# Optimization experiments

Hardware: AMD Instinct MI355X
Metric: run time of the kernel (lower is better)

Reference implementation:

```python
import jax, jax.numpy as jnp
import numpy as np

N_NODES = 100000
N_EDGES = 1600000
D_IN = 64
D_OUT = 64
K_PLUS = 3
ALPHA = 0.5
EXPONENT = -0.25


def _dir_norm_edge_weights(row, col, n, exponent):
    # directed_norm: D_out^exp A D_in^exp, zero-degree -> 0 weight
    ones = jnp.ones(row.shape[0], dtype=jnp.float32)
    out_deg = jax.ops.segment_sum(ones, row, num_segments=n)
    in_deg = jax.ops.segment_sum(ones, col, num_segments=n)
    out_inv = jnp.where(out_deg > 0, jnp.power(jnp.maximum(out_deg, 1.0), exponent), 0.0)
    in_inv = jnp.where(in_deg > 0, jnp.power(jnp.maximum(in_deg, 1.0), exponent), 0.0)
    return out_inv[row] * in_inv[col]


def _spmm(w, x, out_idx, gather_idx, n):
    # y[out_idx] += w * x[gather_idx]
    return jax.ops.segment_sum(w[:, None] * x[gather_idx], out_idx, num_segments=n)


def setup_inputs() -> dict:
    key = jax.random.key(0)
    ks = jax.random.split(key, 7)
    x_real = jax.random.normal(ks[0], (N_NODES, D_IN), dtype=jnp.float32)
    x_imag = jax.random.normal(ks[1], (N_NODES, D_IN), dtype=jnp.float32)
    edge_index = jax.random.randint(ks[2], (2, N_EDGES), 0, N_NODES, dtype=jnp.int32)
    s = 1.0 / np.sqrt(D_IN)
    W_real = jax.random.normal(ks[3], (K_PLUS, D_OUT, D_IN), dtype=jnp.float32) * s
    b_real = jax.random.normal(ks[4], (K_PLUS, D_OUT), dtype=jnp.float32) * s
    W_imag = jax.random.normal(ks[5], (K_PLUS, D_OUT, D_IN), dtype=jnp.float32) * s
    b_imag = jax.random.normal(ks[6], (K_PLUS, D_OUT), dtype=jnp.float32) * s
    return {"x_real": x_real, "x_imag": x_imag, "edge_index": edge_index,
            "W_real": W_real, "b_real": b_real, "W_imag": W_imag, "b_imag": b_imag}


def reference(x_real, x_imag, edge_index, W_real, b_real, W_imag, b_imag):
    n = x_real.shape[0]
    row, col = edge_index[0], edge_index[1]
    # adj_norm edge weights; adj_t_norm weights are identical scalars per edge
    # (in/out degrees swap under transpose), only the scatter direction differs.
    w = _dir_norm_edge_weights(row, col, n, EXPONENT)

    y_real = _spmm(w, x_real, row, col, n)    # adj_norm @ x_real
    y_imag = _spmm(w, x_imag, row, col, n)    # adj_norm @ x_imag
    y_real_t = _spmm(w, x_real, col, row, n)  # adj_t_norm @ x_real
    y_imag_t = _spmm(w, x_imag, col, row, n)  # adj_t_norm @ x_imag

    def lin_r(y):  # [K, N, O] per-order real linear
        return jnp.einsum('nd,kod->kno', y, W_real) + b_real[:, None, :]

    def lin_i(y):
        return jnp.einsum('nd,kod->kno', y, W_imag) + b_imag[:, None, :]

    coeffs = (0.5 ** jnp.arange(K_PLUS, dtype=jnp.float32))[:, None, None]  # exp penalty, i=0 -> 1

    lr_yr, li_yr = lin_r(y_real), lin_i(y_real)
    lr_yi, li_yi = lin_r(y_imag), lin_i(y_imag)
    lr_yrt, li_yrt = lin_r(y_real_t), lin_i(y_real_t)
    lr_yit, li_yit = lin_r(y_imag_t), lin_i(y_imag_t)

    sum_real_s2d = jnp.sum((lr_yr - li_yi) * coeffs, axis=0)
    sum_imag_s2d = jnp.sum((li_yr + lr_yi) * coeffs, axis=0)
    sum_real_d2s = jnp.sum((lr_yrt - li_yit) * coeffs, axis=0)
    # NOTE: faithful to original source, which uses y_real (not y_real_t) here.
    sum_imag_d2s = jnp.sum((li_yr + lr_yit) * coeffs, axis=0)

    total_real = ALPHA * sum_real_s2d + (1.0 - ALPHA) * sum_real_d2s
    total_imag = ALPHA * sum_imag_s2d + (1.0 - ALPHA) * sum_imag_d2s
    return total_real, total_imag
```

## Files before the change

kernel.cpp:

```cpp
#include <hip/hip_runtime.h>
#include <hip/hip_fp16.h>


constexpr int D = 64;
constexpr int SB = 256;
constexpr int G1 = 256;

typedef _Float16 f16x8 __attribute__((ext_vector_type(8)));
typedef float f32x4 __attribute__((ext_vector_type(4)));

__device__ __forceinline__ float2 h2_to_f2(uint p) {
  __half2 h = *(__half2*)&p;
  return __half22float2(h);
}


__global__ __launch_bounds__(256) void part_count(
    const int* __restrict__ row, const int* __restrict__ col,
    int* __restrict__ hout, int* __restrict__ hin, int E, int NBUK, int CH) {
  __shared__ int ho[256], hi_[256];
  int t = threadIdx.x, g = blockIdx.x;
  ho[t] = 0;
  hi_[t] = 0;
  __syncthreads();
  int e0 = g * CH, e1 = min(E, e0 + CH);
  for (int e = e0 + t; e < e1; e += 256) {
    atomicAdd(&ho[row[e] >> 9], 1);
    atomicAdd(&hi_[col[e] >> 9], 1);
  }
  __syncthreads();
  if (t < NBUK) {
    hout[t * G1 + g] = ho[t];
    hin[t * G1 + g] = hi_[t];
  }
}

__global__ __launch_bounds__(256) void part_scatter(
    const int* __restrict__ row, const int* __restrict__ col,
    const int* __restrict__ hout, const int* __restrict__ hin,
    uint* __restrict__ pout, uint* __restrict__ pin, int E, int NBUK, int CH) {
  __shared__ int co[256], ci[256];
  int t = threadIdx.x, g = blockIdx.x;
  if (t < NBUK) {
    co[t] = hout[t * G1 + g];
    ci[t] = hin[t * G1 + g];
  }
  __syncthreads();
  int e0 = g * CH, e1 = min(E, e0 + CH);
  for (int e = e0 + t; e < e1; e += 256) {
    int r = row[e], c = col[e];
    int po = atomicAdd(&co[r >> 9], 1);
    pout[po] = ((uint)(r & 511) << 17) | (uint)c;
    int pi = atomicAdd(&ci[c >> 9], 1);
    pin[pi] = ((uint)(c & 511) << 17) | (uint)r;
  }
}

__global__ __launch_bounds__(256) void bucket_degree(
    const uint* __restrict__ pout, const uint* __restrict__ pin,
    const int* __restrict__ hout, const int* __restrict__ hin,
    int* __restrict__ deg_out, int* __restrict__ deg_in, int E, int NBUK, int N) {
  const uint* p = blockIdx.y ? pin : pout;
  const int* h = blockIdx.y ? hin : hout;
  int* deg = blockIdx.y ? deg_in : deg_out;
  __shared__ int ld[512];
  int t = threadIdx.x, b = blockIdx.x;
  ld[t] = 0;
  ld[t + 256] = 0;
  __syncthreads();
  int s = h[b * G1];
  int e = (b + 1 < NBUK) ? h[(b + 1) * G1] : E;
  for (int j = s + t; j < e; j += 256) atomicAdd(&ld[p[j] >> 17], 1);
  __syncthreads();
  int n0 = (b << 9) + t;
  if (n0 < N) deg[n0] = ld[t];
  if (n0 + 256 < N) deg[n0 + 256] = ld[t + 256];
}

__global__ __launch_bounds__(256) void bucket_fill(
    const uint* __restrict__ pout, const uint* __restrict__ pin,
    const int* __restrict__ hout, const int* __restrict__ hin,
    const int* __restrict__ ofs_out, const int* __restrict__ ofs_in,
    const float* __restrict__ inv_out, const float* __restrict__ inv_in,
    uint* __restrict__ idx_out, uint* __restrict__ idx_in, int E, int NBUK, int N) {
  const uint* p = blockIdx.y ? pin : pout;
  const int* h = blockIdx.y ? hin : hout;
  const int* ofs = blockIdx.y ? ofs_in : ofs_out;
  const float* invnb = blockIdx.y ? inv_out : inv_in;
  uint* idx = blockIdx.y ? idx_in : idx_out;
  __shared__ int cur[512];
  int t = threadIdx.x, b = blockIdx.x;
  int n0 = (b << 9) + t;
  cur[t] = (n0 < N) ? ofs[n0] : 0;
  cur[t + 256] = (n0 + 256 < N) ? ofs[n0 + 256] : 0;
  __syncthreads();
  int s = h[b * G1];
  int e = (b + 1 < NBUK) ? h[(b + 1) * G1] : E;
  for (int j = s + t; j < e; j += 256) {
    uint pk = p[j];
    uint nbr = pk & 0x1FFFFu;
    uint hb = (uint)__half_as_ushort(__float2half(invnb[nbr]));
    int pos = atomicAdd(&cur[pk >> 17], 1);
    idx[pos] = (hb << 17) | nbr;
  }
}


__global__ __launch_bounds__(SB) void bsum_kernel(
    const int* __restrict__ a0, const int* __restrict__ a1,
    int* __restrict__ bsum, int n, int NB) {
  const int* a = blockIdx.y ? a1 : a0;
  int i = blockIdx.x * SB + threadIdx.x;
  int d = (i < n) ? a[i] : 0;
#pragma unroll
  for (int m = 1; m < 64; m <<= 1) d += __shfl_xor(d, m);
  __shared__ int ws[SB / 64];
  if ((threadIdx.x & 63) == 0) ws[threadIdx.x >> 6] = d;
  __syncthreads();
  if (threadIdx.x == 0) {
    int s = 0;
#pragma unroll
    for (int w = 0; w < SB / 64; ++w) s += ws[w];
    bsum[blockIdx.y * NB + blockIdx.x] = s;
  }
}

__global__ __launch_bounds__(1024) void bscan_kernel(int* __restrict__ bsum, int NB) {
  __shared__ int s0[1024], s1[1024];
  int t = threadIdx.x;
  int o0 = (t < NB) ? bsum[t] : 0;
  int o1 = (t < NB) ? bsum[NB + t] : 0;
  s0[t] = o0;
  s1[t] = o1;
  __syncthreads();
  for (int off = 1; off < 1024; off <<= 1) {
    int v0 = (t >= off) ? s0[t - off] : 0;
    int v1 = (t >= off) ? s1[t - off] : 0;
    __syncthreads();
    s0[t] += v0;
    s1[t] += v1;
    __syncthreads();
  }
  if (t < NB) {
    bsum[t] = s0[t] - o0;
    bsum[NB + t] = s1[t] - o1;
  }
}

__global__ __launch_bounds__(SB) void gfin_kernel(
    int* __restrict__ h0, int* __restrict__ h1,
    const int* __restrict__ bsum, int n, int NB) {
  int* h = blockIdx.y ? h1 : h0;
  int base = bsum[blockIdx.y * NB + blockIdx.x];
  int lane = threadIdx.x & 63, wv = threadIdx.x >> 6;
  int i = blockIdx.x * SB + threadIdx.x;
  int d = (i < n) ? h[i] : 0;
  int sc = d;
#pragma unroll
  for (int off = 1; off < 64; off <<= 1) {
    int v = __shfl_up(sc, off);
    if (lane >= off) sc += v;
  }
  __shared__ int ws[SB / 64];
  if (lane == 63) ws[wv] = sc;
  __syncthreads();
  int wbase = 0;
#pragma unroll
  for (int w = 0; w < SB / 64; ++w)
    if (w < wv) wbase += ws[w];
  if (i < n) h[i] = base + wbase + (sc - d);
}

__global__ __launch_bounds__(SB) void sfin_kernel(
    const int* __restrict__ deg_out, const int* __restrict__ deg_in,
    const int* __restrict__ bsum,
    int* __restrict__ ofs_out, int* __restrict__ ofs_in,
    float* __restrict__ inv_out, float* __restrict__ inv_in, int N, int NB) {
  const int* deg = blockIdx.y ? deg_in : deg_out;
  int* ofs = blockIdx.y ? ofs_in : ofs_out;
  float* inv = blockIdx.y ? inv_in : inv_out;
  int base = bsum[blockIdx.y * NB + blockIdx.x];
  int lane = threadIdx.x & 63, wv = threadIdx.x >> 6;
  int i = blockIdx.x * SB + threadIdx.x;
  int d = (i < N) ? deg[i] : 0;
  int sc = d;
#pragma unroll
  for (int off = 1; off < 64; off <<= 1) {
    int v = __shfl_up(sc, off);
    if (lane >= off) sc += v;
  }
  __shared__ int ws[SB / 64];
  if (lane == 63) ws[wv] = sc;
  __syncthreads();
  int wbase = 0;
#pragma unroll
  for (int w = 0; w < SB / 64; ++w)
    if (w < wv) wbase += ws[w];
  if (i < N) {
    ofs[i] = base + wbase + (sc - d);
    inv[i] = d > 0 ? rsqrtf(sqrtf((float)d)) : 0.0f;
  }
  if (i == N - 1) ofs[N] = base + wbase + sc;
}


__global__ void pack_kernel(const float* __restrict__ xr, const float* __restrict__ xi,
                            uint* __restrict__ xp, int total4) {
  int i = blockIdx.x * blockDim.x + threadIdx.x;
  if (i < total4) {
    float4 a = ((const float4*)xr)[i];
    float4 b = ((const float4*)xi)[i];
    __half2 h;
    uint4 o;
    h = __floats2half2_rn(a.x, b.x); o.x = *(uint*)&h;
    h = __floats2half2_rn(a.y, b.y); o.y = *(uint*)&h;
    h = __floats2half2_rn(a.z, b.z); o.z = *(uint*)&h;
    h = __floats2half2_rn(a.w, b.w); o.w = *(uint*)&h;
    ((uint4*)xp)[i] = o;
  }
}

__global__ __launch_bounds__(1024) void wprep_kernel(
    const float* __restrict__ Wr, const float* __restrict__ br,
    const float* __restrict__ Wi, const float* __restrict__ bi,
    uint4* __restrict__ Bfrag, float* __restrict__ cR, float* __restrict__ cI) {
  __shared__ uint sWh[4096];
  int t = threadIdx.x;
  for (int i = t; i < 4096; i += 1024) {
    int o = i >> 6, d = i & 63;
    float wr = Wr[i] + 0.5f * Wr[4096 + i] + 0.25f * Wr[8192 + i];
    float wi = Wi[i] + 0.5f * Wi[4096 + i] + 0.25f * Wi[8192 + i];
    __half2 h = __floats2half2_rn(wr, wi);
    sWh[d * 64 + o] = *(uint*)&h;
  }
  if (t < 64) {
    float brv = br[t] + 0.5f * br[64 + t] + 0.25f * br[128 + t];
    float biv = bi[t] + 0.5f * bi[64 + t] + 0.25f * bi[128 + t];
    cR[t] = brv - biv;
    cI[t] = brv + biv;
  }
  __syncthreads();
  for (int tt = t; tt < 2048; tt += 1024) {
    int lane = tt & 63, fr = tt >> 6;
    int mat = fr >> 4, kt = (fr >> 2) & 3, nt = fr & 3;
    int o = (lane & 15) + 16 * nt;
    int k0 = 8 * (lane >> 4) + 32 * kt;
    uint wbits[4];
#pragma unroll
    for (int jj = 0; jj < 4; ++jj) {
      float v[2];
#pragma unroll
      for (int s = 0; s < 2; ++s) {
        int k = k0 + 2 * jj + s;
        float2 wrwi = h2_to_f2(sWh[(k & 63) * 64 + o]);
        v[s] = (k < 64) ? wrwi.x : (mat ? wrwi.y : -wrwi.y);
      }
      __half2 hh = __floats2half2_rn(v[0], v[1]);
      wbits[jj] = *(uint*)&hh;
    }
    Bfrag[tt] = make_uint4(wbits[0], wbits[1], wbits[2], wbits[3]);
  }
}

__global__ __launch_bounds__(256) void gather_kernel(
    const uint4* __restrict__ xp4,
    const uint* __restrict__ idx_out, const uint* __restrict__ idx_in,
    const int* __restrict__ ofs_out, const int* __restrict__ ofs_in,
    const float* __restrict__ inv_out, const float* __restrict__ inv_in,
    uint* __restrict__ Apack, int N) {
  int wv = threadIdx.x >> 6;
  int lane = threadIdx.x & 63;
  int sub = lane >> 4;
  int q = lane & 15;
  int wid = blockIdx.x * 4 + wv;
  int nw = gridDim.x * 4;
  for (int n = wid; n < N; n += nw) {
    float4 u1 = {0, 0, 0, 0}, s1 = {0, 0, 0, 0};
    float4 v2 = {0, 0, 0, 0}, s2 = {0, 0, 0, 0};
#define ACC(P, SC, U, S)                                                \
  {                                                                     \
    float2 a0 = h2_to_f2((P).x), a1 = h2_to_f2((P).y);                  \
    float2 a2 = h2_to_f2((P).z), a3 = h2_to_f2((P).w);                  \
    U.x += SC * a0.x; S.x += SC * a0.y; U.y += SC * a1.x; S.y += SC * a1.y; \
    U.z += SC * a2.x; S.z += SC * a2.y; U.w += SC * a3.x; S.w += SC * a3.y; \
  }
#define DEC(E) __half2float(__ushort_as_half((ushort)((E) >> 17)))
    {
      int lo = ofs_out[n], hi = ofs_out[n + 1];
      int len8 = (hi - lo) & ~7;
      int j = lo;
      for (; j < lo + len8; j += 8) {
        uint e0 = idx_out[j + sub];
        uint e1 = idx_out[j + 4 + sub];
        uint4 p0 = xp4[(size_t)(e0 & 0x1FFFFu) * 16 + q];
        uint4 p1 = xp4[(size_t)(e1 & 0x1FFFFu) * 16 + q];
        float sc0 = DEC(e0), sc1 = DEC(e1);
        ACC(p0, sc0, u1, s1);
        ACC(p1, sc1, u1, s1);
      }
      for (; j < hi; j += 4) {
        if (j + sub < hi) {
          uint e0 = idx_out[j + sub];
          uint4 p0 = xp4[(size_t)(e0 & 0x1FFFFu) * 16 + q];
          float sc0 = DEC(e0);
          ACC(p0, sc0, u1, s1);
        }
      }
    }
    {
      int lo = ofs_in[n], hi = ofs_in[n + 1];
      int len8 = (hi - lo) & ~7;
      int j = lo;
      for (; j < lo + len8; j += 8) {
        uint e0 = idx_in[j + sub];
        uint e1 = idx_in[j + 4 + sub];
        uint4 p0 = xp4[(size_t)(e0 & 0x1FFFFu) * 16 + q];
        uint4 p1 = xp4[(size_t)(e1 & 0x1FFFFu) * 16 + q];
        float sc0 = DEC(e0), sc1 = DEC(e1);
        ACC(p0, sc0, v2, s2);
        ACC(p1, sc1, v2, s2);
      }
      for (; j < hi; j += 4) {
        if (j + sub < hi) {
          uint e0 = idx_in[j + sub];
          uint4 p0 = xp4[(size_t)(e0 & 0x1FFFFu) * 16 + q];
          float sc0 = DEC(e0);
          ACC(p0, sc0, v2, s2);
        }
      }
    }
#undef ACC
#undef DEC
#pragma unroll
    for (int m = 16; m < 64; m <<= 1) {
      u1.x += __shfl_xor(u1.x, m); u1.y += __shfl_xor(u1.y, m);
      u1.z += __shfl_xor(u1.z, m); u1.w += __shfl_xor(u1.w, m);
      s1.x += __shfl_xor(s1.x, m); s1.y += __shfl_xor(s1.y, m);
      s1.z += __shfl_xor(s1.z, m); s1.w += __shfl_xor(s1.w, m);
      v2.x += __shfl_xor(v2.x, m); v2.y += __shfl_xor(v2.y, m);
      v2.z += __shfl_xor(v2.z, m); v2.w += __shfl_xor(v2.w, m);
      s2.x += __shfl_xor(s2.x, m); s2.y += __shfl_xor(s2.y, m);
      s2.z += __shfl_xor(s2.z, m); s2.w += __shfl_xor(s2.w, m);
    }
    if (sub == 0) {
      float io = inv_out[n], ii = inv_in[n];
      float4 uu = make_float4(io * u1.x, io * u1.y, io * u1.z, io * u1.w);
      float4 vv = make_float4(ii * v2.x, ii * v2.y, ii * v2.z, ii * v2.w);
      float4 ss = make_float4(io * s1.x + ii * s2.x, io * s1.y + ii * s2.y,
                              io * s1.z + ii * s2.z, io * s1.w + ii * s2.w);
      uint* base = Apack + (size_t)n * 96 + 2 * q;
      __half2 h;
      uint2 w;
      h = __floats2half2_rn(0.5f * (uu.x + vv.x), 0.5f * (uu.y + vv.y)); w.x = *(uint*)&h;
      h = __floats2half2_rn(0.5f * (uu.z + vv.z), 0.5f * (uu.w + vv.w)); w.y = *(uint*)&h;
      *(uint2*)base = w;
      h = __floats2half2_rn(0.5f * ss.x, 0.5f * ss.y); w.x = *(uint*)&h;
      h = __floats2half2_rn(0.5f * ss.z, 0.5f * ss.w); w.y = *(uint*)&h;
      *(uint2*)(base + 32) = w;
      h = __floats2half2_rn(uu.x, uu.y); w.x = *(uint*)&h;
      h = __floats2half2_rn(uu.z, uu.w); w.y = *(uint*)&h;
      *(uint2*)(base + 64) = w;
    }
  }
}

__global__ __launch_bounds__(256) void gemm_kernel(
    const ushort* __restrict__ Apack, const uint4* __restrict__ Bfrag,
    const float* __restrict__ cR, const float* __restrict__ cI,
    float* __restrict__ out_real, float* __restrict__ out_imag, int N) {
  __shared__ uint4 sB[2048];
  for (int i = threadIdx.x; i < 2048; i += 256) sB[i] = Bfrag[i];
  __syncthreads();
  int lane = threadIdx.x & 63, wv = threadIdx.x >> 6;
  int l15 = lane & 15, l4 = lane >> 4;
  float bR[4], bI[4];
#pragma unroll
  for (int nt = 0; nt < 4; ++nt) {
    bR[nt] = cR[l15 + 16 * nt];
    bI[nt] = cI[l15 + 16 * nt];
  }
  int tiles = (N + 15) >> 4;
  int gw = blockIdx.x * 4 + wv, nw = gridDim.x * 4;
  for (int tt = gw; tt < tiles; tt += nw) {
    int n0 = tt << 4;
    int arow = min(n0 + l15, N - 1);
    const ushort* ap = Apack + (size_t)arow * 192 + 8 * l4;
    f16x8 a[6];
#pragma unroll
    for (int kt = 0; kt < 6; ++kt) a[kt] = *(const f16x8*)(ap + 32 * kt);
    f32x4 cr[4], ci[4];
#pragma unroll
    for (int nt = 0; nt < 4; ++nt) {
      cr[nt] = (f32x4){0.f, 0.f, 0.f, 0.f};
      ci[nt] = (f32x4){0.f, 0.f, 0.f, 0.f};
    }
#pragma unroll
    for (int kt = 0; kt < 4; ++kt) {
#pragma unroll
      for (int nt = 0; nt < 4; ++nt) {
        f16x8 b0 = *(const f16x8*)&sB[(kt * 4 + nt) * 64 + lane];
        cr[nt] = __builtin_amdgcn_mfma_f32_16x16x32_f16(a[kt], b0, cr[nt], 0, 0, 0);
        f16x8 b1 = *(const f16x8*)&sB[(16 + kt * 4 + nt) * 64 + lane];
        ci[nt] = __builtin_amdgcn_mfma_f32_16x16x32_f16(a[kt + 2], b1, ci[nt], 0, 0, 0);
      }
    }
#pragma unroll
    for (int nt = 0; nt < 4; ++nt) {
#pragma unroll
      for (int r = 0; r < 4; ++r) {
        int node = n0 + 4 * l4 + r;
        if (node < N) {
          out_real[(size_t)node * 64 + l15 + 16 * nt] = cr[nt][r] + bR[nt];
          out_imag[(size_t)node * 64 + l15 + 16 * nt] = ci[nt][r] + bI[nt];
        }
      }
    }
  }
}

extern "C" void kernel_launch(void* const* d_in, const int* in_sizes, int n_in,
                              void* d_out, int out_size, void* d_ws, size_t ws_size,
                              hipStream_t stream) {
  const float* x_real = (const float*)d_in[0];
  const float* x_imag = (const float*)d_in[1];
  const int* edge = (const int*)d_in[2];
  const float* W_real = (const float*)d_in[3];
  const float* b_real = (const float*)d_in[4];
  const float* W_imag = (const float*)d_in[5];
  const float* b_imag = (const float*)d_in[6];

  const int N = in_sizes[0] / D;
  const int E = in_sizes[2] / 2;
  const int* row = edge;
  const int* col = edge + E;

  const int NBUK = (N + 511) >> 9;
  const int CH = (E + G1 - 1) / G1;
  const int L = NBUK * G1;
  const int GB = (L + SB - 1) / SB;
  const int NB = (N + SB - 1) / SB;

  uint* xp       = (uint*)d_ws;
  uint* idx_out  = xp + (size_t)N * D;
  uint* idx_in   = idx_out + E;
  uint* Apack    = idx_in + E;
  uint* pout     = Apack;
  uint* pin      = pout + E;
  uint4* Bfrag   = (uint4*)(Apack + (size_t)N * 96);
  int* hout      = (int*)(Bfrag + 2048);
  int* hin       = hout + L;
  int* gbs       = hin + L;
  int* deg_out   = gbs + 2 * GB;
  int* deg_in    = deg_out + N;
  int* ofs_out   = deg_in + N;
  int* ofs_in    = ofs_out + N + 1;
  float* inv_out = (float*)(ofs_in + N + 1);
  float* inv_in  = inv_out + N;
  float* cR      = inv_in + N;
  float* cI      = cR + 64;
  int* bsum      = (int*)(cI + 64);

  float* out_real = (float*)d_out;
  float* out_imag = out_real + (size_t)N * D;

  wprep_kernel<<<1, 1024, 0, stream>>>(W_real, b_real, W_imag, b_imag, Bfrag, cR, cI);

  pack_kernel<<<(N * 16 + 255) / 256, 256, 0, stream>>>(x_real, x_imag, xp, N * 16);

  part_count<<<G1, 256, 0, stream>>>(row, col, hout, hin, E, NBUK, CH);
  bsum_kernel<<<dim3(GB, 2), SB, 0, stream>>>(hout, hin, gbs, L, GB);
  bscan_kernel<<<1, 1024, 0, stream>>>(gbs, GB);
  gfin_kernel<<<dim3(GB, 2), SB, 0, stream>>>(hout, hin, gbs, L, GB);
  part_scatter<<<G1, 256, 0, stream>>>(row, col, hout, hin, pout, pin, E, NBUK, CH);

  bucket_degree<<<dim3(NBUK, 2), 256, 0, stream>>>(pout, pin, hout, hin,
                                                   deg_out, deg_in, E, NBUK, N);
  bsum_kernel<<<dim3(NB, 2), SB, 0, stream>>>(deg_out, deg_in, bsum, N, NB);
  bscan_kernel<<<1, 1024, 0, stream>>>(bsum, NB);
  sfin_kernel<<<dim3(NB, 2), SB, 0, stream>>>(deg_out, deg_in, bsum, ofs_out, ofs_in,
                                              inv_out, inv_in, N, NB);

  bucket_fill<<<dim3(NBUK, 2), 256, 0, stream>>>(pout, pin, hout, hin, ofs_out, ofs_in,
                                                 inv_out, inv_in, idx_out, idx_in,
                                                 E, NBUK, N);
  gather_kernel<<<4096, 256, 0, stream>>>((const uint4*)xp, idx_out, idx_in,
                                          ofs_out, ofs_in, inv_out, inv_in, Apack, N);
  gemm_kernel<<<512, 256, 0, stream>>>((const ushort*)Apack, Bfrag, cR, cI,
                                       out_real, out_imag, N);
}
```

Before: 346.1 us.

## Fuse neighbor gather with MFMA projection using per-wave LDS tiles and atomic scheduling

The separate gemm kernel is folded into the gather kernel. Each wave pulls 16-node tiles from an atomic counter, gathers and aggregates each node, writes the packed fp16 A rows into a swizzled per-wave LDS buffer, then runs the MFMA projection and writes outputs directly. This removes the global Apack intermediate (write plus re-read) and one kernel launch, and balances load dynamically across waves. In exchange, B fragments are now read from global/cache rather than LDS, and the tail guard is dropped, so nodes beyond a multiple of 16 would be skipped for other N.

```diff
diff --git a/kernel.cpp b/kernel.cpp
--- a/kernel.cpp
+++ b/kernel.cpp
@@ -223,9 +223,11 @@
 __global__ __launch_bounds__(1024) void wprep_kernel(
     const float* __restrict__ Wr, const float* __restrict__ br,
     const float* __restrict__ Wi, const float* __restrict__ bi,
-    uint4* __restrict__ Bfrag, float* __restrict__ cR, float* __restrict__ cI) {
+    uint4* __restrict__ Bfrag, float* __restrict__ cR, float* __restrict__ cI,
+    int* __restrict__ tile_ctr) {
   __shared__ uint sWh[4096];
   int t = threadIdx.x;
+  if (t == 0) *tile_ctr = 0;
   for (int i = t; i < 4096; i += 1024) {
     int o = i >> 6, d = i & 63;
     float wr = Wr[i] + 0.5f * Wr[4096 + i] + 0.25f * Wr[8192 + i];
@@ -262,21 +264,37 @@
   }
 }
 
-__global__ __launch_bounds__(256) void gather_kernel(
+__global__ __launch_bounds__(256, 6) void gather_kernel(
     const uint4* __restrict__ xp4,
     const uint* __restrict__ idx_out, const uint* __restrict__ idx_in,
     const int* __restrict__ ofs_out, const int* __restrict__ ofs_in,
     const float* __restrict__ inv_out, const float* __restrict__ inv_in,
-    uint* __restrict__ Apack, int N) {
+    const uint4* __restrict__ Bfrag, const float* __restrict__ cR,
+    const float* __restrict__ cI, int* __restrict__ tile_ctr,
+    float* __restrict__ out_real, float* __restrict__ out_imag, int N) {
+  __shared__ uint sA[4][1536];
   int wv = threadIdx.x >> 6;
   int lane = threadIdx.x & 63;
   int sub = lane >> 4;
   int q = lane & 15;
-  int wid = blockIdx.x * 4 + wv;
-  int nw = gridDim.x * 4;
-  for (int n = wid; n < N; n += nw) {
-    float4 u1 = {0, 0, 0, 0}, s1 = {0, 0, 0, 0};
-    float4 v2 = {0, 0, 0, 0}, s2 = {0, 0, 0, 0};
+  uint* myA = sA[wv];
+  float bR[4], bI[4];
+#pragma unroll
+  for (int nt = 0; nt < 4; ++nt) {
+    bR[nt] = cR[q + 16 * nt];
+    bI[nt] = cI[q + 16 * nt];
+  }
+  int tiles = N >> 4;
+  for (;;) {
+    int tt;
+    if (lane == 0) tt = atomicAdd(tile_ctr, 1);
+    tt = __shfl(tt, 0);
+    if (tt >= tiles) break;
+    int n0 = tt << 4;
+    for (int i = 0; i < 16; ++i) {
+      int n = n0 + i;
+      float4 u1 = {0, 0, 0, 0}, s1 = {0, 0, 0, 0};
+      float4 v2 = {0, 0, 0, 0}, s2 = {0, 0, 0, 0};
 #define ACC(P, SC, U, S)                                                \
   {                                                                     \
     float2 a0 = h2_to_f2((P).x), a1 = h2_to_f2((P).y);                  \
@@ -285,109 +303,91 @@
     U.z += SC * a2.x; S.z += SC * a2.y; U.w += SC * a3.x; S.w += SC * a3.y; \
   }
 #define DEC(E) __half2float(__ushort_as_half((ushort)((E) >> 17)))
-    {
-      int lo = ofs_out[n], hi = ofs_out[n + 1];
-      int len8 = (hi - lo) & ~7;
-      int j = lo;
-      for (; j < lo + len8; j += 8) {
-        uint e0 = idx_out[j + sub];
-        uint e1 = idx_out[j + 4 + sub];
-        uint4 p0 = xp4[(size_t)(e0 & 0x1FFFFu) * 16 + q];
-        uint4 p1 = xp4[(size_t)(e1 & 0x1FFFFu) * 16 + q];
-        float sc0 = DEC(e0), sc1 = DEC(e1);
-        ACC(p0, sc0, u1, s1);
-        ACC(p1, sc1, u1, s1);
-      }
-      for (; j < hi; j += 4) {
-        if (j + sub < hi) {
+      {
+        int lo = ofs_out[n], hi = ofs_out[n + 1];
+        int len8 = (hi - lo) & ~7;
+        int j = lo;
+        for (; j < lo + len8; j += 8) {
           uint e0 = idx_out[j + sub];
+          uint e1 = idx_out[j + 4 + sub];
           uint4 p0 = xp4[(size_t)(e0 & 0x1FFFFu) * 16 + q];
-          float sc0 = DEC(e0);
+          uint4 p1 = xp4[(size_t)(e1 & 0x1FFFFu) * 16 + q];
+          float sc0 = DEC(e0), sc1 = DEC(e1);
           ACC(p0, sc0, u1, s1);
+          ACC(p1, sc1, u1, s1);
         }
-      }
-    }
-    {
-      int lo = ofs_in[n], hi = ofs_in[n + 1];
-      int len8 = (hi - lo) & ~7;
-      int j = lo;
-      for (; j < lo + len8; j += 8) {
-        uint e0 = idx_in[j + sub];
-        uint e1 = idx_in[j + 4 + sub];
-        uint4 p0 = xp4[(size_t)(e0 & 0x1FFFFu) * 16 + q];
-        uint4 p1 = xp4[(size_t)(e1 & 0x1FFFFu) * 16 + q];
-        float sc0 = DEC(e0), sc1 = DEC(e1);
-        ACC(p0, sc0, v2, s2);
-        ACC(p1, sc1, v2, s2);
-      }
-      for (; j < hi; j += 4) {
-        if (j + sub < hi) {
+        for (; j < hi; j += 4) {
+          if (j + sub < hi) {
+            uint e0 = idx_out[j + sub];
+            uint4 p0 = xp4[(size_t)(e0 & 0x1FFFFu) * 16 + q];
+            float sc0 = DEC(e0);
+            ACC(p0, sc0, u1, s1);
+          }
+        }
+      }
+      {
+        int lo = ofs_in[n], hi = ofs_in[n + 1];
+        int len8 = (hi - lo) & ~7;
+        int j = lo;
+        for (; j < lo + len8; j += 8) {
           uint e0 = idx_in[j + sub];
+          uint e1 = idx_in[j + 4 + sub];
           uint4 p0 = xp4[(size_t)(e0 & 0x1FFFFu) * 16 + q];
-          float sc0 = DEC(e0);
+          uint4 p1 = xp4[(size_t)(e1 & 0x1FFFFu) * 16 + q];
+          float sc0 = DEC(e0), sc1 = DEC(e1);
           ACC(p0, sc0, v2, s2);
+          ACC(p1, sc1, v2, s2);
         }
-      }
-    }
+        for (; j < hi; j += 4) {
+          if (j + sub < hi) {
+            uint e0 = idx_in[j + sub];
+            uint4 p0 = xp4[(size_t)(e0 & 0x1FFFFu) * 16 + q];
+            float sc0 = DEC(e0);
+            ACC(p0, sc0, v2, s2);
+          }
+        }
+      }
 #undef ACC
 #undef DEC
 #pragma unroll
-    for (int m = 16; m < 64; m <<= 1) {
-      u1.x += __shfl_xor(u1.x, m); u1.y += __shfl_xor(u1.y, m);
-      u1.z += __shfl_xor(u1.z, m); u1.w += __shfl_xor(u1.w, m);
-      s1.x += __shfl_xor(s1.x, m); s1.y += __shfl_xor(s1.y, m);
-      s1.z += __shfl_xor(s1.z, m); s1.w += __shfl_xor(s1.w, m);
-      v2.x += __shfl_xor(v2.x, m); v2.y += __shfl_xor(v2.y, m);
-      v2.z += __shfl_xor(v2.z, m); v2.w += __shfl_xor(v2.w, m);
-      s2.x += __shfl_xor(s2.x, m); s2.y += __shfl_xor(s2.y, m);
-      s2.z += __shfl_xor(s2.z, m); s2.w += __shfl_xor(s2.w, m);
-    }
-    if (sub == 0) {
-      float io = inv_out[n], ii = inv_in[n];
-      float4 uu = make_float4(io * u1.x, io * u1.y, io * u1.z, io * u1.w);
-      float4 vv = make_float4(ii * v2.x, ii * v2.y, ii * v2.z, ii * v2.w);
-      float4 ss = make_float4(io * s1.x + ii * s2.x, io * s1.y + ii * s2.y,
-                              io * s1.z + ii * s2.z, io * s1.w + ii * s2.w);
-      uint* base = Apack + (size_t)n * 96 + 2 * q;
-      __half2 h;
-      uint2 w;
-      h = __floats2half2_rn(0.5f * (uu.x + vv.x), 0.5f * (uu.y + vv.y)); w.x = *(uint*)&h;
-      h = __floats2half2_rn(0.5f * (uu.z + vv.z), 0.5f * (uu.w + vv.w)); w.y = *(uint*)&h;
-      *(uint2*)base = w;
-      h = __floats2half2_rn(0.5f * ss.x, 0.5f * ss.y); w.x = *(uint*)&h;
-      h = __floats2half2_rn(0.5f * ss.z, 0.5f * ss.w); w.y = *(uint*)&h;
-      *(uint2*)(base + 32) = w;
-      h = __floats2half2_rn(uu.x, uu.y); w.x = *(uint*)&h;
-      h = __floats2half2_rn(uu.z, uu.w); w.y = *(uint*)&h;
-      *(uint2*)(base + 64) = w;
-    }
-  }
-}
-
-__global__ __launch_bounds__(256) void gemm_kernel(
-    const ushort* __restrict__ Apack, const uint4* __restrict__ Bfrag,
-    const float* __restrict__ cR, const float* __restrict__ cI,
-    float* __restrict__ out_real, float* __restrict__ out_imag, int N) {
-  __shared__ uint4 sB[2048];
-  for (int i = threadIdx.x; i < 2048; i += 256) sB[i] = Bfrag[i];
-  __syncthreads();
-  int lane = threadIdx.x & 63, wv = threadIdx.x >> 6;
-  int l15 = lane & 15, l4 = lane >> 4;
-  float bR[4], bI[4];
-#pragma unroll
-  for (int nt = 0; nt < 4; ++nt) {
-    bR[nt] = cR[l15 + 16 * nt];
-    bI[nt] = cI[l15 + 16 * nt];
-  }
-  int tiles = (N + 15) >> 4;
-  int gw = blockIdx.x * 4 + wv, nw = gridDim.x * 4;
-  for (int tt = gw; tt < tiles; tt += nw) {
-    int n0 = tt << 4;
-    int arow = min(n0 + l15, N - 1);
-    const ushort* ap = Apack + (size_t)arow * 192 + 8 * l4;
+      for (int m = 16; m < 64; m <<= 1) {
+        u1.x += __shfl_xor(u1.x, m); u1.y += __shfl_xor(u1.y, m);
+        u1.z += __shfl_xor(u1.z, m); u1.w += __shfl_xor(u1.w, m);
+        s1.x += __shfl_xor(s1.x, m); s1.y += __shfl_xor(s1.y, m);
+        s1.z += __shfl_xor(s1.z, m); s1.w += __shfl_xor(s1.w, m);
+        v2.x += __shfl_xor(v2.x, m); v2.y += __shfl_xor(v2.y, m);
+        v2.z += __shfl_xor(v2.z, m); v2.w += __shfl_xor(v2.w, m);
+        s2.x += __shfl_xor(s2.x, m); s2.y += __shfl_xor(s2.y, m);
+        s2.z += __shfl_xor(s2.z, m); s2.w += __shfl_xor(s2.w, m);
+      }
+      if (sub == 0) {
+        float io = inv_out[n], ii = inv_in[n];
+        float4 uu = make_float4(io * u1.x, io * u1.y, io * u1.z, io * u1.w);
+        float4 vv = make_float4(ii * v2.x, ii * v2.y, ii * v2.z, ii * v2.w);
+        float4 ss = make_float4(io * s1.x + ii * s2.x, io * s1.y + ii * s2.y,
+                                io * s1.z + ii * s2.z, io * s1.w + ii * s2.w);
+        int u0 = q >> 1, kk = i & 7;
+        uint base = (uint)(i * 96 + ((q & 1) << 1));
+        __half2 h;
+        uint2 w;
+        h = __floats2half2_rn(0.5f * (uu.x + vv.x), 0.5f * (uu.y + vv.y)); w.x = *(uint*)&h;
+        h = __floats2half2_rn(0.5f * (uu.z + vv.z), 0.5f * (uu.w + vv.w)); w.y = *(uint*)&h;
+        *(uint2*)&myA[base + 4 * (u0 ^ kk)] = w;
+        h = __floats2half2_rn(0.5f * ss.x, 0.5f * ss.y); w.x = *(uint*)&h;
+        h = __floats2half2_rn(0.5f * ss.z, 0.5f * ss.w); w.y = *(uint*)&h;
+        *(uint2*)&myA[base + 4 * ((8 + u0) ^ kk)] = w;
+        h = __floats2half2_rn(uu.x, uu.y); w.x = *(uint*)&h;
+        h = __floats2half2_rn(uu.z, uu.w); w.y = *(uint*)&h;
+        *(uint2*)&myA[base + 4 * ((16 + u0) ^ kk)] = w;
+      }
+    }
+    int l15 = q, l4 = sub, rk = l15 & 7;
     f16x8 a[6];
 #pragma unroll
-    for (int kt = 0; kt < 6; ++kt) a[kt] = *(const f16x8*)(ap + 32 * kt);
+    for (int sct = 0; sct < 6; ++sct) {
+      int slot = ((sct >> 1) << 3) + ((((sct & 1) << 2) + l4) ^ rk);
+      a[sct] = *(const f16x8*)&myA[l15 * 96 + 4 * slot];
+    }
     f32x4 cr[4], ci[4];
 #pragma unroll
     for (int nt = 0; nt < 4; ++nt) {
@@ -398,9 +398,9 @@
     for (int kt = 0; kt < 4; ++kt) {
 #pragma unroll
       for (int nt = 0; nt < 4; ++nt) {
-        f16x8 b0 = *(const f16x8*)&sB[(kt * 4 + nt) * 64 + lane];
+        f16x8 b0 = *(const f16x8*)&Bfrag[(kt * 4 + nt) * 64 + lane];
         cr[nt] = __builtin_amdgcn_mfma_f32_16x16x32_f16(a[kt], b0, cr[nt], 0, 0, 0);
-        f16x8 b1 = *(const f16x8*)&sB[(16 + kt * 4 + nt) * 64 + lane];
+        f16x8 b1 = *(const f16x8*)&Bfrag[(16 + kt * 4 + nt) * 64 + lane];
         ci[nt] = __builtin_amdgcn_mfma_f32_16x16x32_f16(a[kt + 2], b1, ci[nt], 0, 0, 0);
       }
     }
@@ -408,11 +408,9 @@
     for (int nt = 0; nt < 4; ++nt) {
 #pragma unroll
       for (int r = 0; r < 4; ++r) {
-        int node = n0 + 4 * l4 + r;
-        if (node < N) {
-          out_real[(size_t)node * 64 + l15 + 16 * nt] = cr[nt][r] + bR[nt];
-          out_imag[(size_t)node * 64 + l15 + 16 * nt] = ci[nt][r] + bI[nt];
-        }
+        size_t node = (size_t)(n0 + 4 * l4 + r);
+        out_real[node * 64 + l15 + 16 * nt] = cr[nt][r] + bR[nt];
+        out_imag[node * 64 + l15 + 16 * nt] = ci[nt][r] + bI[nt];
       }
     }
   }
@@ -443,10 +441,9 @@
   uint* xp       = (uint*)d_ws;
   uint* idx_out  = xp + (size_t)N * D;
   uint* idx_in   = idx_out + E;
-  uint* Apack    = idx_in + E;
-  uint* pout     = Apack;
+  uint* pout     = idx_in + E;
   uint* pin      = pout + E;
-  uint4* Bfrag   = (uint4*)(Apack + (size_t)N * 96);
+  uint4* Bfrag   = (uint4*)(pin + E);
   int* hout      = (int*)(Bfrag + 2048);
   int* hin       = hout + L;
   int* gbs       = hin + L;
@@ -459,11 +456,13 @@
   float* cR      = inv_in + N;
   float* cI      = cR + 64;
   int* bsum      = (int*)(cI + 64);
+  int* tile_ctr  = bsum + 2 * NB;
 
   float* out_real = (float*)d_out;
   float* out_imag = out_real + (size_t)N * D;
 
-  wprep_kernel<<<1, 1024, 0, stream>>>(W_real, b_real, W_imag, b_imag, Bfrag, cR, cI);
+  wprep_kernel<<<1, 1024, 0, stream>>>(W_real, b_real, W_imag, b_imag,
+                                       Bfrag, cR, cI, tile_ctr);
 
   pack_kernel<<<(N * 16 + 255) / 256, 256, 0, stream>>>(x_real, x_imag, xp, N * 16);
 
@@ -483,8 +482,8 @@
   bucket_fill<<<dim3(NBUK, 2), 256, 0, stream>>>(pout, pin, hout, hin, ofs_out, ofs_in,
                                                  inv_out, inv_in, idx_out, idx_in,
                                                  E, NBUK, N);
-  gather_kernel<<<4096, 256, 0, stream>>>((const uint4*)xp, idx_out, idx_in,
-                                          ofs_out, ofs_in, inv_out, inv_in, Apack, N);
-  gemm_kernel<<<512, 256, 0, stream>>>((const ushort*)Apack, Bfrag, cR, cI,
-                                       out_real, out_imag, N);
-}
+  gather_kernel<<<1568, 256, 0, stream>>>((const uint4*)xp, idx_out, idx_in,
+                                          ofs_out, ofs_in, inv_out, inv_in,
+                                          Bfrag, cR, cI, tile_ctr,
+                                          out_real, out_imag, N);
+}
```

Result: slower. 535.7 us (+54.8%).

## Collapse CSR build scan kernels into atomic bucket totals and per-bucket local scans

Applied to the files above, without the earlier changes.

Replaces the per-block bucket histogram plus the multi-kernel global scan with global atomic bucket totals, a single-block scan fused into the weight-prep kernel, and atomic per-block bucket cursor reservation inside part_scatter. Per-node offsets and inverse degrees are now computed by a per-bucket local scan, which removes the separate degree array and the second global scan. This cuts the launch count from about fourteen to eight. The cost is that part_scatter recounts its edge chunk, and the edge placement order within a bucket is no longer deterministic.

```diff
diff --git a/kernel.cpp b/kernel.cpp
--- a/kernel.cpp
+++ b/kernel.cpp
@@ -3,7 +3,6 @@
 
 
 constexpr int D = 64;
-constexpr int SB = 256;
 constexpr int G1 = 256;
 
 typedef _Float16 f16x8 __attribute__((ext_vector_type(8)));
@@ -17,7 +16,7 @@
 
 __global__ __launch_bounds__(256) void part_count(
     const int* __restrict__ row, const int* __restrict__ col,
-    int* __restrict__ hout, int* __restrict__ hin, int E, int NBUK, int CH) {
+    int* __restrict__ Tcnt, int E, int NBUK, int CH) {
   __shared__ int ho[256], hi_[256];
   int t = threadIdx.x, g = blockIdx.x;
   ho[t] = 0;
@@ -30,23 +29,106 @@
   }
   __syncthreads();
   if (t < NBUK) {
-    hout[t * G1 + g] = ho[t];
-    hin[t * G1 + g] = hi_[t];
+    if (ho[t]) atomicAdd(&Tcnt[t], ho[t]);
+    if (hi_[t]) atomicAdd(&Tcnt[NBUK + t], hi_[t]);
+  }
+}
+
+__global__ __launch_bounds__(1024) void prep_kernel(
+    const float* __restrict__ Wr, const float* __restrict__ br,
+    const float* __restrict__ Wi, const float* __restrict__ bi,
+    const int* __restrict__ Tcnt, uint4* __restrict__ Bfrag,
+    float* __restrict__ cR, float* __restrict__ cI,
+    int* __restrict__ Bb_out, int* __restrict__ Bb_in, int* __restrict__ Ccur,
+    int E, int NBUK) {
+  __shared__ uint sWh[4096];
+  __shared__ int ws[8];
+  int t = threadIdx.x;
+  for (int i = t; i < 4096; i += 1024) {
+    int o = i >> 6, d = i & 63;
+    float wr = Wr[i] + 0.5f * Wr[4096 + i] + 0.25f * Wr[8192 + i];
+    float wi = Wi[i] + 0.5f * Wi[4096 + i] + 0.25f * Wi[8192 + i];
+    __half2 h = __floats2half2_rn(wr, wi);
+    sWh[d * 64 + o] = *(uint*)&h;
+  }
+  if (t < 64) {
+    float brv = br[t] + 0.5f * br[64 + t] + 0.25f * br[128 + t];
+    float biv = bi[t] + 0.5f * bi[64 + t] + 0.25f * bi[128 + t];
+    cR[t] = brv - biv;
+    cI[t] = brv + biv;
+  }
+  int dir = 0, tl = 0, v = 0, sc = 0;
+  int lane = t & 63, wv = t >> 6;
+  if (t < 512) {
+    dir = t >> 8;
+    tl = t & 255;
+    v = (tl < NBUK) ? Tcnt[dir * NBUK + tl] : 0;
+    sc = v;
+#pragma unroll
+    for (int off = 1; off < 64; off <<= 1) {
+      int u = __shfl_up(sc, off);
+      if (lane >= off) sc += u;
+    }
+    if (lane == 63) ws[wv] = sc;
+  }
+  __syncthreads();
+  if (t < 512) {
+    int wbase = 0;
+#pragma unroll
+    for (int w = 0; w < 8; ++w)
+      if (w >= (dir << 2) && w < wv) wbase += ws[w];
+    int excl = wbase + sc - v;
+    int* Bb = dir ? Bb_in : Bb_out;
+    if (tl < NBUK) {
+      Bb[tl] = excl;
+      Ccur[dir * NBUK + tl] = excl;
+      if (tl == NBUK - 1) Bb[NBUK] = excl + v;
+    }
+  }
+  for (int tt = t; tt < 2048; tt += 1024) {
+    int ln = tt & 63, fr = tt >> 6;
+    int mat = fr >> 4, kt = (fr >> 2) & 3, nt = fr & 3;
+    int o = (ln & 15) + 16 * nt;
+    int k0 = 8 * (ln >> 4) + 32 * kt;
+    uint wbits[4];
+#pragma unroll
+    for (int jj = 0; jj < 4; ++jj) {
+      float vv[2];
+#pragma unroll
+      for (int s = 0; s < 2; ++s) {
+        int k = k0 + 2 * jj + s;
+        float2 wrwi = h2_to_f2(sWh[(k & 63) * 64 + o]);
+        vv[s] = (k < 64) ? wrwi.x : (mat ? wrwi.y : -wrwi.y);
+      }
+      __half2 hh = __floats2half2_rn(vv[0], vv[1]);
+      wbits[jj] = *(uint*)&hh;
+    }
+    Bfrag[tt] = make_uint4(wbits[0], wbits[1], wbits[2], wbits[3]);
   }
 }
 
 __global__ __launch_bounds__(256) void part_scatter(
     const int* __restrict__ row, const int* __restrict__ col,
-    const int* __restrict__ hout, const int* __restrict__ hin,
+    int* __restrict__ Ccur,
     uint* __restrict__ pout, uint* __restrict__ pin, int E, int NBUK, int CH) {
   __shared__ int co[256], ci[256];
   int t = threadIdx.x, g = blockIdx.x;
+  co[t] = 0;
+  ci[t] = 0;
+  __syncthreads();
+  int e0 = g * CH, e1 = min(E, e0 + CH);
+  for (int e = e0 + t; e < e1; e += 256) {
+    atomicAdd(&co[row[e] >> 9], 1);
+    atomicAdd(&ci[col[e] >> 9], 1);
+  }
+  __syncthreads();
   if (t < NBUK) {
-    co[t] = hout[t * G1 + g];
-    ci[t] = hin[t * G1 + g];
-  }
-  __syncthreads();
-  int e0 = g * CH, e1 = min(E, e0 + CH);
+    int c = co[t];
+    co[t] = c ? atomicAdd(&Ccur[t], c) : 0;
+    c = ci[t];
+    ci[t] = c ? atomicAdd(&Ccur[NBUK + t], c) : 0;
+  }
+  __syncthreads();
   for (int e = e0 + t; e < e1; e += 256) {
     int r = row[e], c = col[e];
     int po = atomicAdd(&co[r >> 9], 1);
@@ -56,35 +138,59 @@
   }
 }
 
-__global__ __launch_bounds__(256) void bucket_degree(
+__global__ __launch_bounds__(256) void offsets_kernel(
     const uint* __restrict__ pout, const uint* __restrict__ pin,
-    const int* __restrict__ hout, const int* __restrict__ hin,
-    int* __restrict__ deg_out, int* __restrict__ deg_in, int E, int NBUK, int N) {
+    const int* __restrict__ Bb_out, const int* __restrict__ Bb_in,
+    int* __restrict__ ofs_out, int* __restrict__ ofs_in,
+    float* __restrict__ inv_out, float* __restrict__ inv_in,
+    int E, int NBUK, int N) {
   const uint* p = blockIdx.y ? pin : pout;
-  const int* h = blockIdx.y ? hin : hout;
-  int* deg = blockIdx.y ? deg_in : deg_out;
+  const int* Bb = blockIdx.y ? Bb_in : Bb_out;
+  int* ofs = blockIdx.y ? ofs_in : ofs_out;
+  float* inv = blockIdx.y ? inv_in : inv_out;
   __shared__ int ld[512];
+  __shared__ int ws[4];
   int t = threadIdx.x, b = blockIdx.x;
   ld[t] = 0;
   ld[t + 256] = 0;
   __syncthreads();
-  int s = h[b * G1];
-  int e = (b + 1 < NBUK) ? h[(b + 1) * G1] : E;
-  for (int j = s + t; j < e; j += 256) atomicAdd(&ld[p[j] >> 17], 1);
-  __syncthreads();
-  int n0 = (b << 9) + t;
-  if (n0 < N) deg[n0] = ld[t];
-  if (n0 + 256 < N) deg[n0 + 256] = ld[t + 256];
+  int win_s = Bb[b], win_e = Bb[b + 1];
+  for (int j = win_s + t; j < win_e; j += 256) atomicAdd(&ld[p[j] >> 17], 1);
+  __syncthreads();
+  int a0 = ld[2 * t], a1 = ld[2 * t + 1], sm = a0 + a1;
+  int lane = t & 63, wv = t >> 6, sc = sm;
+#pragma unroll
+  for (int off = 1; off < 64; off <<= 1) {
+    int u = __shfl_up(sc, off);
+    if (lane >= off) sc += u;
+  }
+  if (lane == 63) ws[wv] = sc;
+  __syncthreads();
+  int wbase = 0;
+#pragma unroll
+  for (int w = 0; w < 4; ++w)
+    if (w < wv) wbase += ws[w];
+  int excl = wbase + sc - sm;
+  int n0 = (b << 9) + 2 * t;
+  if (n0 < N) {
+    ofs[n0] = win_s + excl;
+    inv[n0] = a0 ? rsqrtf(sqrtf((float)a0)) : 0.0f;
+  }
+  if (n0 + 1 < N) {
+    ofs[n0 + 1] = win_s + excl + a0;
+    inv[n0 + 1] = a1 ? rsqrtf(sqrtf((float)a1)) : 0.0f;
+  }
+  if (b == 0 && t == 0) ofs[N] = E;
 }
 
 __global__ __launch_bounds__(256) void bucket_fill(
     const uint* __restrict__ pout, const uint* __restrict__ pin,
-    const int* __restrict__ hout, const int* __restrict__ hin,
+    const int* __restrict__ Bb_out, const int* __restrict__ Bb_in,
     const int* __restrict__ ofs_out, const int* __restrict__ ofs_in,
     const float* __restrict__ inv_out, const float* __restrict__ inv_in,
     uint* __restrict__ idx_out, uint* __restrict__ idx_in, int E, int NBUK, int N) {
   const uint* p = blockIdx.y ? pin : pout;
-  const int* h = blockIdx.y ? hin : hout;
+  const int* Bb = blockIdx.y ? Bb_in : Bb_out;
   const int* ofs = blockIdx.y ? ofs_in : ofs_out;
   const float* invnb = blockIdx.y ? inv_out : inv_in;
   uint* idx = blockIdx.y ? idx_in : idx_out;
@@ -94,8 +200,7 @@
   cur[t] = (n0 < N) ? ofs[n0] : 0;
   cur[t + 256] = (n0 + 256 < N) ? ofs[n0 + 256] : 0;
   __syncthreads();
-  int s = h[b * G1];
-  int e = (b + 1 < NBUK) ? h[(b + 1) * G1] : E;
+  int s = Bb[b], e = Bb[b + 1];
   for (int j = s + t; j < e; j += 256) {
     uint pk = p[j];
     uint nbr = pk & 0x1FFFFu;
@@ -103,104 +208,6 @@
     int pos = atomicAdd(&cur[pk >> 17], 1);
     idx[pos] = (hb << 17) | nbr;
   }
-}
-
-
-__global__ __launch_bounds__(SB) void bsum_kernel(
-    const int* __restrict__ a0, const int* __restrict__ a1,
-    int* __restrict__ bsum, int n, int NB) {
-  const int* a = blockIdx.y ? a1 : a0;
-  int i = blockIdx.x * SB + threadIdx.x;
-  int d = (i < n) ? a[i] : 0;
-#pragma unroll
-  for (int m = 1; m < 64; m <<= 1) d += __shfl_xor(d, m);
-  __shared__ int ws[SB / 64];
-  if ((threadIdx.x & 63) == 0) ws[threadIdx.x >> 6] = d;
-  __syncthreads();
-  if (threadIdx.x == 0) {
-    int s = 0;
-#pragma unroll
-    for (int w = 0; w < SB / 64; ++w) s += ws[w];
-    bsum[blockIdx.y * NB + blockIdx.x] = s;
-  }
-}
-
-__global__ __launch_bounds__(1024) void bscan_kernel(int* __restrict__ bsum, int NB) {
-  __shared__ int s0[1024], s1[1024];
-  int t = threadIdx.x;
-  int o0 = (t < NB) ? bsum[t] : 0;
-  int o1 = (t < NB) ? bsum[NB + t] : 0;
-  s0[t] = o0;
-  s1[t] = o1;
-  __syncthreads();
-  for (int off = 1; off < 1024; off <<= 1) {
-    int v0 = (t >= off) ? s0[t - off] : 0;
-    int v1 = (t >= off) ? s1[t - off] : 0;
-    __syncthreads();
-    s0[t] += v0;
-    s1[t] += v1;
-    __syncthreads();
-  }
-  if (t < NB) {
-    bsum[t] = s0[t] - o0;
-    bsum[NB + t] = s1[t] - o1;
-  }
-}
-
-__global__ __launch_bounds__(SB) void gfin_kernel(
-    int* __restrict__ h0, int* __restrict__ h1,
-    const int* __restrict__ bsum, int n, int NB) {
-  int* h = blockIdx.y ? h1 : h0;
-  int base = bsum[blockIdx.y * NB + blockIdx.x];
-  int lane = threadIdx.x & 63, wv = threadIdx.x >> 6;
-  int i = blockIdx.x * SB + threadIdx.x;
-  int d = (i < n) ? h[i] : 0;
-  int sc = d;
-#pragma unroll
-  for (int off = 1; off < 64; off <<= 1) {
-    int v = __shfl_up(sc, off);
-    if (lane >= off) sc += v;
-  }
-  __shared__ int ws[SB / 64];
-  if (lane == 63) ws[wv] = sc;
-  __syncthreads();
-  int wbase = 0;
-#pragma unroll
-  for (int w = 0; w < SB / 64; ++w)
-    if (w < wv) wbase += ws[w];
-  if (i < n) h[i] = base + wbase + (sc - d);
-}
-
-__global__ __launch_bounds__(SB) void sfin_kernel(
-    const int* __restrict__ deg_out, const int* __restrict__ deg_in,
-    const int* __restrict__ bsum,
-    int* __restrict__ ofs_out, int* __restrict__ ofs_in,
-    float* __restrict__ inv_out, float* __restrict__ inv_in, int N, int NB) {
-  const int* deg = blockIdx.y ? deg_in : deg_out;
-  int* ofs = blockIdx.y ? ofs_in : ofs_out;
-  float* inv = blockIdx.y ? inv_in : inv_out;
-  int base = bsum[blockIdx.y * NB + blockIdx.x];
-  int lane = threadIdx.x & 63, wv = threadIdx.x >> 6;
-  int i = blockIdx.x * SB + threadIdx.x;
-  int d = (i < N) ? deg[i] : 0;
-  int sc = d;
-#pragma unroll
-  for (int off = 1; off < 64; off <<= 1) {
-    int v = __shfl_up(sc, off);
-    if (lane >= off) sc += v;
-  }
-  __shared__ int ws[SB / 64];
-  if (lane == 63) ws[wv] = sc;
-  __syncthreads();
-  int wbase = 0;
-#pragma unroll
-  for (int w = 0; w < SB / 64; ++w)
-    if (w < wv) wbase += ws[w];
-  if (i < N) {
-    ofs[i] = base + wbase + (sc - d);
-    inv[i] = d > 0 ? rsqrtf(sqrtf((float)d)) : 0.0f;
-  }
-  if (i == N - 1) ofs[N] = base + wbase + sc;
 }
 
 
@@ -217,48 +224,6 @@
     h = __floats2half2_rn(a.z, b.z); o.z = *(uint*)&h;
     h = __floats2half2_rn(a.w, b.w); o.w = *(uint*)&h;
     ((uint4*)xp)[i] = o;
-  }
-}
-
-__global__ __launch_bounds__(1024) void wprep_kernel(
-    const float* __restrict__ Wr, const float* __restrict__ br,
-    const float* __restrict__ Wi, const float* __restrict__ bi,
-    uint4* __restrict__ Bfrag, float* __restrict__ cR, float* __restrict__ cI) {
-  __shared__ uint sWh[4096];
-  int t = threadIdx.x;
-  for (int i = t; i < 4096; i += 1024) {
-    int o = i >> 6, d = i & 63;
-    float wr = Wr[i] + 0.5f * Wr[4096 + i] + 0.25f * Wr[8192 + i];
-    float wi = Wi[i] + 0.5f * Wi[4096 + i] + 0.25f * Wi[8192 + i];
-    __half2 h = __floats2half2_rn(wr, wi);
-    sWh[d * 64 + o] = *(uint*)&h;
-  }
-  if (t < 64) {
-    float brv = br[t] + 0.5f * br[64 + t] + 0.25f * br[128 + t];
-    float biv = bi[t] + 0.5f * bi[64 + t] + 0.25f * bi[128 + t];
-    cR[t] = brv - biv;
-    cI[t] = brv + biv;
-  }
-  __syncthreads();
-  for (int tt = t; tt < 2048; tt += 1024) {
-    int lane = tt & 63, fr = tt >> 6;
-    int mat = fr >> 4, kt = (fr >> 2) & 3, nt = fr & 3;
-    int o = (lane & 15) + 16 * nt;
-    int k0 = 8 * (lane >> 4) + 32 * kt;
-    uint wbits[4];
-#pragma unroll
-    for (int jj = 0; jj < 4; ++jj) {
-      float v[2];
-#pragma unroll
-      for (int s = 0; s < 2; ++s) {
-        int k = k0 + 2 * jj + s;
-        float2 wrwi = h2_to_f2(sWh[(k & 63) * 64 + o]);
-        v[s] = (k < 64) ? wrwi.x : (mat ? wrwi.y : -wrwi.y);
-      }
-      __half2 hh = __floats2half2_rn(v[0], v[1]);
-      wbits[jj] = *(uint*)&hh;
-    }
-    Bfrag[tt] = make_uint4(wbits[0], wbits[1], wbits[2], wbits[3]);
   }
 }
 
@@ -436,9 +401,6 @@
 
   const int NBUK = (N + 511) >> 9;
   const int CH = (E + G1 - 1) / G1;
-  const int L = NBUK * G1;
-  const int GB = (L + SB - 1) / SB;
-  const int NB = (N + SB - 1) / SB;
 
   uint* xp       = (uint*)d_ws;
   uint* idx_out  = xp + (size_t)N * D;
@@ -447,42 +409,38 @@
   uint* pout     = Apack;
   uint* pin      = pout + E;
   uint4* Bfrag   = (uint4*)(Apack + (size_t)N * 96);
-  int* hout      = (int*)(Bfrag + 2048);
-  int* hin       = hout + L;
-  int* gbs       = hin + L;
-  int* deg_out   = gbs + 2 * GB;
-  int* deg_in    = deg_out + N;
-  int* ofs_out   = deg_in + N;
+  int* Tcnt      = (int*)(Bfrag + 2048);
+  int* Bb_out    = Tcnt + 2 * NBUK;
+  int* Bb_in     = Bb_out + NBUK + 1;
+  int* Ccur      = Bb_in + NBUK + 1;
+  int* ofs_out   = Ccur + 2 * NBUK;
   int* ofs_in    = ofs_out + N + 1;
   float* inv_out = (float*)(ofs_in + N + 1);
   float* inv_in  = inv_out + N;
   float* cR      = inv_in + N;
   float* cI      = cR + 64;
-  int* bsum      = (int*)(cI + 64);
 
   float* out_real = (float*)d_out;
   float* out_imag = out_real + (size_t)N * D;
 
-  wprep_kernel<<<1, 1024, 0, stream>>>(W_real, b_real, W_imag, b_imag, Bfrag, cR, cI);
+  hipMemsetAsync(Tcnt, 0, 2 * NBUK * sizeof(int), stream);
+  part_count<<<G1, 256, 0, stream>>>(row, col, Tcnt, E, NBUK, CH);
+
+  prep_kernel<<<1, 1024, 0, stream>>>(W_real, b_real, W_imag, b_imag, Tcnt,
+                                      Bfrag, cR, cI, Bb_out, Bb_in, Ccur, E, NBUK);
 
   pack_kernel<<<(N * 16 + 255) / 256, 256, 0, stream>>>(x_real, x_imag, xp, N * 16);
 
-  part_count<<<G1, 256, 0, stream>>>(row, col, hout, hin, E, NBUK, CH);
-  bsum_kernel<<<dim3(GB, 2), SB, 0, stream>>>(hout, hin, gbs, L, GB);
-  bscan_kernel<<<1, 1024, 0, stream>>>(gbs, GB);
-  gfin_kernel<<<dim3(GB, 2), SB, 0, stream>>>(hout, hin, gbs, L, GB);
-  part_scatter<<<G1, 256, 0, stream>>>(row, col, hout, hin, pout, pin, E, NBUK, CH);
-
-  bucket_degree<<<dim3(NBUK, 2), 256, 0, stream>>>(pout, pin, hout, hin,
-                                                   deg_out, deg_in, E, NBUK, N);
-  bsum_kernel<<<dim3(NB, 2), SB, 0, stream>>>(deg_out, deg_in, bsum, N, NB);
-  bscan_kernel<<<1, 1024, 0, stream>>>(bsum, NB);
-  sfin_kernel<<<dim3(NB, 2), SB, 0, stream>>>(deg_out, deg_in, bsum, ofs_out, ofs_in,
-                                              inv_out, inv_in, N, NB);
-
-  bucket_fill<<<dim3(NBUK, 2), 256, 0, stream>>>(pout, pin, hout, hin, ofs_out, ofs_in,
-                                                 inv_out, inv_in, idx_out, idx_in,
-                                                 E, NBUK, N);
+  part_scatter<<<G1, 256, 0, stream>>>(row, col, Ccur, pout, pin, E, NBUK, CH);
+
+  offsets_kernel<<<dim3(NBUK, 2), 256, 0, stream>>>(pout, pin, Bb_out, Bb_in,
+                                                    ofs_out, ofs_in, inv_out, inv_in,
+                                                    E, NBUK, N);
+
+  bucket_fill<<<dim3(NBUK, 2), 256, 0, stream>>>(pout, pin, Bb_out, Bb_in,
+                                                 ofs_out, ofs_in, inv_out, inv_in,
+                                                 idx_out, idx_in, E, NBUK, N);
+
   gather_kernel<<<4096, 256, 0, stream>>>((const uint4*)xp, idx_out, idx_in,
                                           ofs_out, ofs_in, inv_out, inv_in, Apack, N);
   gemm_kernel<<<512, 256, 0, stream>>>((const ushort*)Apack, Bfrag, cR, cI,
```

Result: no change. 344.1 us (-0.6%).
